# Kernel optimization log

Measured on AMD Instinct MI355X. Metric: run time of the kernel, lower is better.

The kernel has to match this reference:

```python
import jax, jax.numpy as jnp
import numpy as np

B, S, H = 2, 2048, 1024
E, K, F = 64, 8, 512
NORM_TOPK = True
CAP_FACTOR = 2.0


def setup_inputs() -> dict:
    key = jax.random.key(0)
    k0, k1, k2, k3, k4 = jax.random.split(key, 5)
    s_h = 1.0 / np.sqrt(H)
    s_f = 1.0 / np.sqrt(F)
    return {
        "hidden_states": jax.random.normal(k0, (B, S, H), jnp.float32),
        "w_gate": jax.random.normal(k1, (H, E), jnp.float32) * s_h,  # gate: Linear(H->E), no bias
        "w1": jax.random.normal(k2, (E, H, F), jnp.float32) * s_h,   # gate_proj per expert
        "w3": jax.random.normal(k3, (E, H, F), jnp.float32) * s_h,   # up_proj per expert
        "w2": jax.random.normal(k4, (E, F, H), jnp.float32) * s_f,   # down_proj per expert
    }


def reference(hidden_states, w_gate, w1, w3, w2):
    b, s, h = hidden_states.shape
    e = w_gate.shape[1]
    t = b * s
    x = hidden_states.reshape(t, h)
    router_logits = x @ w_gate                                   # [T, E]
    probs = jax.nn.softmax(router_logits.astype(jnp.float32), axis=-1)
    topw, sel = jax.lax.top_k(probs, K)                          # [T, K]
    if NORM_TOPK:
        topw = topw / jnp.sum(topw, axis=-1, keepdims=True)
    topw = topw.astype(x.dtype)

    a = t * K                                                    # total assignments
    c = int(CAP_FACTOR * a / e)                                  # static per-expert capacity
    sel_flat = sel.reshape(a)
    w_flat = topw.reshape(a)
    tok = jnp.repeat(jnp.arange(t), K)
    order = jnp.argsort(sel_flat, stable=True)                   # group assignments by expert
    e_s, t_s, w_s = sel_flat[order], tok[order], w_flat[order]
    counts = jnp.bincount(sel_flat, length=e)
    starts = jnp.cumsum(counts) - counts
    pos = jnp.arange(a) - starts[e_s]                            # position within expert group
    valid = pos < c
    slot = jnp.where(valid, e_s * c + pos, e * c)                # overflow -> dropped sentinel slot

    # dispatch: gather tokens into per-expert contiguous buffer [E, C, H]
    buf = jnp.zeros((e * c + 1, h), x.dtype).at[slot].set(x[t_s])
    xb = buf[: e * c].reshape(e, c, h)
    # grouped gated-SiLU MLP per expert
    g = jnp.einsum('ech,ehf->ecf', xb, w1)
    u = jnp.einsum('ech,ehf->ecf', xb, w3)
    yb = jnp.einsum('ecf,efh->ech', jax.nn.silu(g) * u, w2).reshape(e * c, h)
    # combine: weighted scatter-add back to tokens
    contrib = yb[jnp.minimum(slot, e * c - 1)] * (w_s * valid.astype(x.dtype))[:, None]
    out = jnp.zeros((t, h), x.dtype).at[t_s].add(contrib)
    return out.reshape(b, s, h), router_logits
```

## Files before the change

kernel.cpp:

```cpp
#include <hip/hip_runtime.h>
#include <hip/hip_bf16.h>

#define T_TOK 4096
#define H_DIM 1024
#define E_EXP 64
#define TOPK  8
#define F_DIM 512
#define CAP   1024
#define A_TOT (T_TOK * TOPK)

typedef _Float16 f16;
typedef _Float16 f16x2 __attribute__((ext_vector_type(2)));
typedef _Float16 f16x8 __attribute__((ext_vector_type(8)));
typedef float    f32x4 __attribute__((ext_vector_type(4)));

__global__ __launch_bounds__(256) void pack_w_kernel(
    const float* __restrict__ src, f16* __restrict__ dst, int Kd, int Nd)
{
    const int lane = threadIdx.x & 63;
    const int wv   = threadIdx.x >> 6;
    const int nt_cnt = Nd >> 4, kt_cnt = Kd >> 5;
    int chunk = blockIdx.x * 4 + wv;
    int nt = chunk % nt_cnt;
    int kt = (chunk / nt_cnt) % kt_cnt;
    int e  = chunk / (nt_cnt * kt_cnt);
    const float* s = src + ((size_t)e * Kd + kt * 32 + (lane >> 4) * 8) * Nd
                         + nt * 16 + (lane & 15);
    f16x8 v;
    #pragma unroll
    for (int j = 0; j < 8; ++j) v[j] = (f16)s[(size_t)j * Nd];
    size_t dchunk = ((size_t)e * nt_cnt + nt) * kt_cnt + kt;
    *(f16x8*)(dst + dchunk * 512 + lane * 8) = v;
}

__global__ __launch_bounds__(256) void router_kernel(
    const float* __restrict__ x, const float* __restrict__ wg,
    float* __restrict__ logits_out, int* __restrict__ sel,
    float* __restrict__ wgtA, f16* __restrict__ xh)
{
    __shared__ float xs[16][128];
    __shared__ float ls[16][65];
    const int tid = threadIdx.x;
    const int e  = tid & 63;
    const int tg = tid >> 6;
    const int tb = blockIdx.x * 16;

    float acc[4] = {0.f, 0.f, 0.f, 0.f};
    for (int h0 = 0; h0 < H_DIM; h0 += 128) {
        {
            int r  = tid >> 4;
            int c0 = (tid & 15) * 8;
            const float4* src = (const float4*)(x + (size_t)(tb + r) * H_DIM + h0 + c0);
            float4 v0 = src[0], v1 = src[1];
            *(float4*)&xs[r][c0]     = v0;
            *(float4*)&xs[r][c0 + 4] = v1;
            f16x8 hv;
            hv[0] = (f16)v0.x; hv[1] = (f16)v0.y; hv[2] = (f16)v0.z; hv[3] = (f16)v0.w;
            hv[4] = (f16)v1.x; hv[5] = (f16)v1.y; hv[6] = (f16)v1.z; hv[7] = (f16)v1.w;
            *(f16x8*)(xh + (size_t)(tb + r) * H_DIM + h0 + c0) = hv;
        }
        __syncthreads();
        for (int hh = 0; hh < 128; ++hh) {
            float w = wg[(size_t)(h0 + hh) * E_EXP + e];
            #pragma unroll
            for (int i = 0; i < 4; ++i)
                acc[i] = fmaf(xs[tg * 4 + i][hh], w, acc[i]);
        }
        __syncthreads();
    }
    #pragma unroll
    for (int i = 0; i < 4; ++i) {
        int tt = tg * 4 + i;
        logits_out[(size_t)(tb + tt) * E_EXP + e] = acc[i];
        ls[tt][e] = acc[i];
    }
    __syncthreads();
    if (tid < 16) {
        int tt = tid;
        float lv[8]; int li[8];
        for (int k = 0; k < 8; ++k) {
            float m = -1e30f; int mi = 0;
            for (int j = 0; j < 64; ++j) {
                float v = ls[tt][j];
                if (v > m) { m = v; mi = j; }
            }
            lv[k] = m; li[k] = mi;
            ls[tt][mi] = -1e30f;
        }
        float s = 0.f, wv[8];
        for (int k = 0; k < 8; ++k) { wv[k] = __expf(lv[k] - lv[0]); s += wv[k]; }
        float inv = 1.f / s;
        for (int k = 0; k < 8; ++k) {
            int a = (tb + tt) * TOPK + k;
            sel[a]  = li[k];
            wgtA[a] = wv[k] * inv;
        }
    }
}

__global__ __launch_bounds__(256) void build_lists_kernel(
    const int* __restrict__ sel, const float* __restrict__ wgtA,
    int* __restrict__ tok_list, float* __restrict__ wgt_list,
    int* __restrict__ counts)
{
    __shared__ int sc[256];
    const int e = blockIdx.x;
    const int tid = threadIdx.x;
    const int per = A_TOT / 256;
    const int a0 = tid * per;
    int cnt = 0;
    for (int i = 0; i < per; ++i) cnt += (sel[a0 + i] == e) ? 1 : 0;
    sc[tid] = cnt;
    __syncthreads();
    for (int s = 1; s < 256; s <<= 1) {
        int v = (tid >= s) ? sc[tid - s] : 0;
        __syncthreads();
        sc[tid] += v;
        __syncthreads();
    }
    int total = sc[255];
    int pos = sc[tid] - cnt;
    if (tid == 0) counts[e] = (total < CAP) ? total : CAP;
    for (int i = 0; i < per; ++i) {
        int a = a0 + i;
        if (sel[a] == e) {
            if (pos < CAP) {
                tok_list[e * CAP + pos] = a >> 3;
                wgt_list[e * CAP + pos] = wgtA[a];
            }
            pos++;
        }
    }
}

#define MFMA16(a, b, c) __builtin_amdgcn_mfma_f32_16x16x32_f16(a, b, c, 0, 0, 0)

__global__ __launch_bounds__(256) void gemm1_kernel(
    const f16* __restrict__ xh, const f16* __restrict__ w1p,
    const f16* __restrict__ w3p, const int* __restrict__ tok_list,
    const int* __restrict__ counts, f16* __restrict__ P)
{
    const int id = blockIdx.x;
    const int rest = id >> 3;
    const int g  = (id & 7) + ((rest >> 4) << 3);
    const int m0 = (rest & 15) * 64;
    const int bf = (g & 7) * 64;
    const int e  = g >> 3;
    const int cnt = counts[e];
    if (m0 >= cnt) return;

    __shared__ f16 Xs[64][72];
    __shared__ int tok_s[64];

    const int tid = threadIdx.x;
    const int lane = tid & 63, wv = tid >> 6;
    const int jj = lane & 15, qq = lane >> 4;

    if (tid < 64) {
        int m = m0 + tid;
        tok_s[tid] = (m < cnt) ? tok_list[e * CAP + m] : tok_list[e * CAP];
    }
    __syncthreads();

    const int sr = tid >> 3, sc = (tid & 7) * 8;

    const f16* w1b = w1p + ((size_t)e * 32 + (bf >> 4) + wv) * 32 * 512 + lane * 8;
    const f16* w3b = w3p + ((size_t)e * 32 + (bf >> 4) + wv) * 32 * 512 + lane * 8;

    f32x4 accG[4], accU[4];
    #pragma unroll
    for (int i = 0; i < 4; ++i) {
        accG[i] = (f32x4){0.f, 0.f, 0.f, 0.f};
        accU[i] = (f32x4){0.f, 0.f, 0.f, 0.f};
    }

    f16x8 pG0 = *(const f16x8*)(w1b);
    f16x8 pG1 = *(const f16x8*)(w1b + 512);
    f16x8 pU0 = *(const f16x8*)(w3b);
    f16x8 pU1 = *(const f16x8*)(w3b + 512);

    for (int k0 = 0; k0 < H_DIM; k0 += 64) {
        f16x8 x0 = *(const f16x8*)(xh + (size_t)tok_s[sr]      * H_DIM + k0 + sc);
        f16x8 x1 = *(const f16x8*)(xh + (size_t)tok_s[sr + 32] * H_DIM + k0 + sc);
        __syncthreads();
        *(f16x8*)&Xs[sr][sc]      = x0;
        *(f16x8*)&Xs[sr + 32][sc] = x1;
        __syncthreads();
        f16x8 cG0 = pG0, cG1 = pG1, cU0 = pU0, cU1 = pU1;
        if (k0 + 64 < H_DIM) {
            size_t kg = (size_t)((k0 >> 5) + 2) * 512;
            pG0 = *(const f16x8*)(w1b + kg);
            pG1 = *(const f16x8*)(w1b + kg + 512);
            pU0 = *(const f16x8*)(w3b + kg);
            pU1 = *(const f16x8*)(w3b + kg + 512);
        }
        #pragma unroll
        for (int mt = 0; mt < 4; ++mt) {
            f16x8 a0 = *(const f16x8*)&Xs[mt * 16 + jj][qq * 8];
            f16x8 a1 = *(const f16x8*)&Xs[mt * 16 + jj][32 + qq * 8];
            accG[mt] = MFMA16(a0, cG0, accG[mt]);
            accU[mt] = MFMA16(a0, cU0, accU[mt]);
            accG[mt] = MFMA16(a1, cG1, accG[mt]);
            accU[mt] = MFMA16(a1, cU1, accU[mt]);
        }
    }
    #pragma unroll
    for (int mt = 0; mt < 4; ++mt) {
        #pragma unroll
        for (int r = 0; r < 4; ++r) {
            int row = mt * 16 + qq * 4 + r;
            float gg = accG[mt][r], u = accU[mt][r];
            float p = gg / (1.f + __expf(-gg)) * u;
            P[(size_t)(e * CAP + m0 + row) * F_DIM + bf + wv * 16 + jj] = (f16)p;
        }
    }
}

__global__ __launch_bounds__(256) void gemm2_kernel(
    const f16* __restrict__ P, const f16* __restrict__ w2p,
    const int* __restrict__ tok_list, const float* __restrict__ wgt_list,
    const int* __restrict__ counts, float* __restrict__ out)
{
    const int id = blockIdx.x;
    const int rest = id >> 3;
    const int g  = (id & 7) + ((rest >> 4) << 3);
    const int m0 = (rest & 15) * 64;
    const int h0 = (g & 15) * 64;
    const int e  = g >> 4;
    const int cnt = counts[e];
    if (m0 >= cnt) return;

    __shared__ f16   Ps[64][72];
    __shared__ int   tok_s[64];
    __shared__ float wgt_s[64];

    const int tid = threadIdx.x;
    const int lane = tid & 63, wv = tid >> 6;
    const int jj = lane & 15, qq = lane >> 4;

    if (tid < 64) {
        int m = m0 + tid;
        tok_s[tid] = (m < cnt) ? tok_list[e * CAP + m] : 0;
        wgt_s[tid] = (m < cnt) ? wgt_list[e * CAP + m] : 0.f;
    }

    const int sr = tid >> 3, sc = (tid & 7) * 8;
    const size_t pbase = (size_t)(e * CAP + m0) * F_DIM;

    const f16* w2b = w2p + ((size_t)e * 64 + (h0 >> 4) + wv) * 16 * 512 + lane * 8;

    f32x4 acc[4];
    #pragma unroll
    for (int i = 0; i < 4; ++i) acc[i] = (f32x4){0.f, 0.f, 0.f, 0.f};

    f16x8 p0 = *(const f16x8*)(w2b);
    f16x8 p1 = *(const f16x8*)(w2b + 512);

    for (int k0 = 0; k0 < F_DIM; k0 += 64) {
        f16x8 x0 = *(const f16x8*)(P + pbase + (size_t)sr        * F_DIM + k0 + sc);
        f16x8 x1 = *(const f16x8*)(P + pbase + (size_t)(sr + 32) * F_DIM + k0 + sc);
        __syncthreads();
        *(f16x8*)&Ps[sr][sc]      = x0;
        *(f16x8*)&Ps[sr + 32][sc] = x1;
        __syncthreads();
        f16x8 c0 = p0, c1 = p1;
        if (k0 + 64 < F_DIM) {
            size_t kg = (size_t)((k0 >> 5) + 2) * 512;
            p0 = *(const f16x8*)(w2b + kg);
            p1 = *(const f16x8*)(w2b + kg + 512);
        }
        #pragma unroll
        for (int mt = 0; mt < 4; ++mt) {
            f16x8 a0 = *(const f16x8*)&Ps[mt * 16 + jj][qq * 8];
            f16x8 a1 = *(const f16x8*)&Ps[mt * 16 + jj][32 + qq * 8];
            acc[mt] = MFMA16(a0, c0, acc[mt]);
            acc[mt] = MFMA16(a1, c1, acc[mt]);
        }
    }
    #pragma unroll
    for (int mt = 0; mt < 4; ++mt) {
        #pragma unroll
        for (int r = 0; r < 4; ++r) {
            int row = mt * 16 + qq * 4 + r;
            if (m0 + row < cnt) {
                float y = acc[mt][r] * wgt_s[row];
                unsafeAtomicAdd(&out[(size_t)tok_s[row] * H_DIM + h0 + wv * 16 + jj], y);
            }
        }
    }
}

extern "C" void kernel_launch(void* const* d_in, const int* in_sizes, int n_in,
                              void* d_out, int out_size, void* d_ws, size_t ws_size,
                              hipStream_t stream) {
    const float* x  = (const float*)d_in[0];
    const float* wg = (const float*)d_in[1];
    const float* w1 = (const float*)d_in[2];
    const float* w3 = (const float*)d_in[3];
    const float* w2 = (const float*)d_in[4];

    float* out    = (float*)d_out;
    float* logits = out + (size_t)T_TOK * H_DIM;

    char* ws = (char*)d_ws;
    int*   sel      = (int*)  (ws);
    float* wgtA     = (float*)(ws + (128 << 10));
    int*   tok_list = (int*)  (ws + (256 << 10));
    float* wgt_list = (float*)(ws + (512 << 10));
    int*   counts   = (int*)  (ws + (768 << 10));
    f16*   xh       = (f16*)  (ws + (size_t)(1 << 20));
    f16*   P        = (f16*)  (ws + (size_t)(9 << 20));
    f16*   w1p      = (f16*)  (ws + (size_t)(73 << 20));
    f16*   w3p      = (f16*)  (ws + (size_t)(137 << 20));
    f16*   w2p      = (f16*)  (ws + (size_t)(201 << 20));

    hipMemsetAsync(out, 0, (size_t)T_TOK * H_DIM * sizeof(float), stream);
    pack_w_kernel<<<16384, 256, 0, stream>>>(w1, w1p, H_DIM, F_DIM);
    pack_w_kernel<<<16384, 256, 0, stream>>>(w3, w3p, H_DIM, F_DIM);
    pack_w_kernel<<<16384, 256, 0, stream>>>(w2, w2p, F_DIM, H_DIM);
    router_kernel<<<T_TOK / 16, 256, 0, stream>>>(x, wg, logits, sel, wgtA, xh);
    build_lists_kernel<<<E_EXP, 256, 0, stream>>>(sel, wgtA, tok_list, wgt_list, counts);
    gemm1_kernel<<<16 * 8 * E_EXP, 256, 0, stream>>>(xh, w1p, w3p, tok_list, counts, P);
    gemm2_kernel<<<16 * 16 * E_EXP, 256, 0, stream>>>(P, w2p, tok_list, wgt_list, counts, out);
}
```

Baseline: 742.8 us.

## Coalesce weight packing via LDS tile, double-buffer GEMM tiles, widen gemm2 N-tile

The weight pack kernel now reads rows of the fp32 weights with float4 loads into an LDS tile and transposes them from there, instead of doing strided scalar loads per lane. Both expert GEMMs double-buffer the activation tile in shared memory, which drops one barrier per k-step and overlaps the next global load with the MFMA work. gemm2 now computes a 128-wide output tile per block, with two accumulator sets per wave, halving its grid and the number of times each P tile is reloaded. Block-index decoding is remapped in both GEMMs, which changes how blocks are scheduled; the cost is more registers and LDS per block.

Result: faster. 711.3 us (-4.2%).

```diff
diff --git a/kernel.cpp b/kernel.cpp
--- a/kernel.cpp
+++ b/kernel.cpp
@@ -11,26 +11,44 @@
 
 typedef _Float16 f16;
 typedef _Float16 f16x2 __attribute__((ext_vector_type(2)));
+typedef _Float16 f16x4 __attribute__((ext_vector_type(4)));
 typedef _Float16 f16x8 __attribute__((ext_vector_type(8)));
 typedef float    f32x4 __attribute__((ext_vector_type(4)));
 
 __global__ __launch_bounds__(256) void pack_w_kernel(
     const float* __restrict__ src, f16* __restrict__ dst, int Kd, int Nd)
 {
-    const int lane = threadIdx.x & 63;
-    const int wv   = threadIdx.x >> 6;
-    const int nt_cnt = Nd >> 4, kt_cnt = Kd >> 5;
-    int chunk = blockIdx.x * 4 + wv;
-    int nt = chunk % nt_cnt;
-    int kt = (chunk / nt_cnt) % kt_cnt;
-    int e  = chunk / (nt_cnt * kt_cnt);
-    const float* s = src + ((size_t)e * Kd + kt * 32 + (lane >> 4) * 8) * Nd
-                         + nt * 16 + (lane & 15);
-    f16x8 v;
-    #pragma unroll
-    for (int j = 0; j < 8; ++j) v[j] = (f16)s[(size_t)j * Nd];
-    size_t dchunk = ((size_t)e * nt_cnt + nt) * kt_cnt + kt;
-    *(f16x8*)(dst + dchunk * 512 + lane * 8) = v;
+    __shared__ f16 tile[32][132];
+    const int tid = threadIdx.x;
+    const int nb = Nd >> 7;
+    const int kb = Kd >> 5;
+    const int b = blockIdx.x;
+    const int n0  = (b % nb) * 128;
+    const int kt0 = (b / nb) % kb;
+    const int e   = b / (nb * kb);
+
+    const float* s = src + ((size_t)e * Kd + kt0 * 32) * Nd + n0;
+    #pragma unroll
+    for (int rep = 0; rep < 4; ++rep) {
+        int idx = rep * 256 + tid;
+        int r = idx >> 5, c = (idx & 31) * 4;
+        float4 v = *(const float4*)(s + (size_t)r * Nd + c);
+        f16x4 h; h[0] = (f16)v.x; h[1] = (f16)v.y; h[2] = (f16)v.z; h[3] = (f16)v.w;
+        *(f16x4*)&tile[r][c] = h;
+    }
+    __syncthreads();
+    const int lane = tid & 63, wv = tid >> 6;
+    #pragma unroll
+    for (int ci = 0; ci < 2; ++ci) {
+        int c = wv + ci * 4;
+        f16x8 v;
+        #pragma unroll
+        for (int j = 0; j < 8; ++j)
+            v[j] = tile[(lane >> 4) * 8 + j][c * 16 + (lane & 15)];
+        int nt = (n0 >> 4) + c;
+        size_t chunk = ((size_t)e * (Nd >> 4) + nt) * kb + kt0;
+        *(f16x8*)(dst + chunk * 512 + lane * 8) = v;
+    }
 }
 
 __global__ __launch_bounds__(256) void router_kernel(
@@ -141,31 +159,32 @@
     const int* __restrict__ counts, f16* __restrict__ P)
 {
     const int id = blockIdx.x;
-    const int rest = id >> 3;
-    const int g  = (id & 7) + ((rest >> 4) << 3);
-    const int m0 = (rest & 15) * 64;
-    const int bf = (g & 7) * 64;
-    const int e  = g >> 3;
+    const int x7 = id & 7, r = id >> 3;
+    const int ft = r & 7, mt = (r >> 3) & 15, eh = r >> 7;
+    const int e = x7 + 8 * eh;
     const int cnt = counts[e];
+    const int m0 = mt * 64;
     if (m0 >= cnt) return;
-
-    __shared__ f16 Xs[64][72];
+    const int bf = ft * 64;
+
+    __shared__ f16 Xs[2][64][72];
     __shared__ int tok_s[64];
 
     const int tid = threadIdx.x;
     const int lane = tid & 63, wv = tid >> 6;
     const int jj = lane & 15, qq = lane >> 4;
+    const int sr = tid >> 3, sc = (tid & 7) * 8;
 
     if (tid < 64) {
         int m = m0 + tid;
         tok_s[tid] = (m < cnt) ? tok_list[e * CAP + m] : tok_list[e * CAP];
     }
     __syncthreads();
-
-    const int sr = tid >> 3, sc = (tid & 7) * 8;
-
-    const f16* w1b = w1p + ((size_t)e * 32 + (bf >> 4) + wv) * 32 * 512 + lane * 8;
-    const f16* w3b = w3p + ((size_t)e * 32 + (bf >> 4) + wv) * 32 * 512 + lane * 8;
+    const size_t rowA = (size_t)tok_s[sr] * H_DIM + sc;
+    const size_t rowB = (size_t)tok_s[sr + 32] * H_DIM + sc;
+
+    const f16* w1b = w1p + (((size_t)e * 32 + ft * 4 + wv) * 32) * 512 + lane * 8;
+    const f16* w3b = w3p + (((size_t)e * 32 + ft * 4 + wv) * 32) * 512 + lane * 8;
 
     f32x4 accG[4], accU[4];
     #pragma unroll
@@ -174,42 +193,53 @@
         accU[i] = (f32x4){0.f, 0.f, 0.f, 0.f};
     }
 
-    f16x8 pG0 = *(const f16x8*)(w1b);
-    f16x8 pG1 = *(const f16x8*)(w1b + 512);
-    f16x8 pU0 = *(const f16x8*)(w3b);
-    f16x8 pU1 = *(const f16x8*)(w3b + 512);
-
-    for (int k0 = 0; k0 < H_DIM; k0 += 64) {
-        f16x8 x0 = *(const f16x8*)(xh + (size_t)tok_s[sr]      * H_DIM + k0 + sc);
-        f16x8 x1 = *(const f16x8*)(xh + (size_t)tok_s[sr + 32] * H_DIM + k0 + sc);
-        __syncthreads();
-        *(f16x8*)&Xs[sr][sc]      = x0;
-        *(f16x8*)&Xs[sr + 32][sc] = x1;
-        __syncthreads();
-        f16x8 cG0 = pG0, cG1 = pG1, cU0 = pU0, cU1 = pU1;
-        if (k0 + 64 < H_DIM) {
-            size_t kg = (size_t)((k0 >> 5) + 2) * 512;
-            pG0 = *(const f16x8*)(w1b + kg);
-            pG1 = *(const f16x8*)(w1b + kg + 512);
-            pU0 = *(const f16x8*)(w3b + kg);
-            pU1 = *(const f16x8*)(w3b + kg + 512);
-        }
-        #pragma unroll
-        for (int mt = 0; mt < 4; ++mt) {
-            f16x8 a0 = *(const f16x8*)&Xs[mt * 16 + jj][qq * 8];
-            f16x8 a1 = *(const f16x8*)&Xs[mt * 16 + jj][32 + qq * 8];
-            accG[mt] = MFMA16(a0, cG0, accG[mt]);
-            accU[mt] = MFMA16(a0, cU0, accU[mt]);
-            accG[mt] = MFMA16(a1, cG1, accG[mt]);
-            accU[mt] = MFMA16(a1, cU1, accU[mt]);
-        }
-    }
-    #pragma unroll
-    for (int mt = 0; mt < 4; ++mt) {
-        #pragma unroll
-        for (int r = 0; r < 4; ++r) {
-            int row = mt * 16 + qq * 4 + r;
-            float gg = accG[mt][r], u = accU[mt][r];
+    {
+        f16x8 a = *(const f16x8*)(xh + rowA);
+        f16x8 b = *(const f16x8*)(xh + rowB);
+        *(f16x8*)&Xs[0][sr][sc]      = a;
+        *(f16x8*)&Xs[0][sr + 32][sc] = b;
+    }
+    f16x8 cG0 = *(const f16x8*)(w1b);
+    f16x8 cG1 = *(const f16x8*)(w1b + 512);
+    f16x8 cU0 = *(const f16x8*)(w3b);
+    f16x8 cU1 = *(const f16x8*)(w3b + 512);
+
+    #pragma unroll
+    for (int it = 0; it < 16; ++it) {
+        const int k0 = it * 64;
+        __syncthreads();
+        f16x8 xn0, xn1, nG0, nG1, nU0, nU1;
+        if (it < 15) {
+            xn0 = *(const f16x8*)(xh + rowA + k0 + 64);
+            xn1 = *(const f16x8*)(xh + rowB + k0 + 64);
+            size_t kg = (size_t)(2 * it + 2) * 512;
+            nG0 = *(const f16x8*)(w1b + kg);
+            nG1 = *(const f16x8*)(w1b + kg + 512);
+            nU0 = *(const f16x8*)(w3b + kg);
+            nU1 = *(const f16x8*)(w3b + kg + 512);
+        }
+        const int buf = it & 1;
+        #pragma unroll
+        for (int m2 = 0; m2 < 4; ++m2) {
+            f16x8 a0 = *(const f16x8*)&Xs[buf][m2 * 16 + jj][qq * 8];
+            f16x8 a1 = *(const f16x8*)&Xs[buf][m2 * 16 + jj][32 + qq * 8];
+            accG[m2] = MFMA16(a0, cG0, accG[m2]);
+            accU[m2] = MFMA16(a0, cU0, accU[m2]);
+            accG[m2] = MFMA16(a1, cG1, accG[m2]);
+            accU[m2] = MFMA16(a1, cU1, accU[m2]);
+        }
+        if (it < 15) {
+            *(f16x8*)&Xs[buf ^ 1][sr][sc]      = xn0;
+            *(f16x8*)&Xs[buf ^ 1][sr + 32][sc] = xn1;
+            cG0 = nG0; cG1 = nG1; cU0 = nU0; cU1 = nU1;
+        }
+    }
+    #pragma unroll
+    for (int m2 = 0; m2 < 4; ++m2) {
+        #pragma unroll
+        for (int rr = 0; rr < 4; ++rr) {
+            int row = m2 * 16 + qq * 4 + rr;
+            float gg = accG[m2][rr], u = accU[m2][rr];
             float p = gg / (1.f + __expf(-gg)) * u;
             P[(size_t)(e * CAP + m0 + row) * F_DIM + bf + wv * 16 + jj] = (f16)p;
         }
@@ -222,21 +252,22 @@
     const int* __restrict__ counts, float* __restrict__ out)
 {
     const int id = blockIdx.x;
-    const int rest = id >> 3;
-    const int g  = (id & 7) + ((rest >> 4) << 3);
-    const int m0 = (rest & 15) * 64;
-    const int h0 = (g & 15) * 64;
-    const int e  = g >> 4;
+    const int x7 = id & 7, r = id >> 3;
+    const int ht = r & 7, mt = (r >> 3) & 15, eh = r >> 7;
+    const int e = x7 + 8 * eh;
     const int cnt = counts[e];
+    const int m0 = mt * 64;
     if (m0 >= cnt) return;
-
-    __shared__ f16   Ps[64][72];
+    const int h0 = ht * 128;
+
+    __shared__ f16   Ps[2][64][72];
     __shared__ int   tok_s[64];
     __shared__ float wgt_s[64];
 
     const int tid = threadIdx.x;
     const int lane = tid & 63, wv = tid >> 6;
     const int jj = lane & 15, qq = lane >> 4;
+    const int sr = tid >> 3, sc = (tid & 7) * 8;
 
     if (tid < 64) {
         int m = m0 + tid;
@@ -244,47 +275,68 @@
         wgt_s[tid] = (m < cnt) ? wgt_list[e * CAP + m] : 0.f;
     }
 
-    const int sr = tid >> 3, sc = (tid & 7) * 8;
     const size_t pbase = (size_t)(e * CAP + m0) * F_DIM;
-
-    const f16* w2b = w2p + ((size_t)e * 64 + (h0 >> 4) + wv) * 16 * 512 + lane * 8;
-
-    f32x4 acc[4];
-    #pragma unroll
-    for (int i = 0; i < 4; ++i) acc[i] = (f32x4){0.f, 0.f, 0.f, 0.f};
-
-    f16x8 p0 = *(const f16x8*)(w2b);
-    f16x8 p1 = *(const f16x8*)(w2b + 512);
-
-    for (int k0 = 0; k0 < F_DIM; k0 += 64) {
-        f16x8 x0 = *(const f16x8*)(P + pbase + (size_t)sr        * F_DIM + k0 + sc);
-        f16x8 x1 = *(const f16x8*)(P + pbase + (size_t)(sr + 32) * F_DIM + k0 + sc);
-        __syncthreads();
-        *(f16x8*)&Ps[sr][sc]      = x0;
-        *(f16x8*)&Ps[sr + 32][sc] = x1;
-        __syncthreads();
-        f16x8 c0 = p0, c1 = p1;
-        if (k0 + 64 < F_DIM) {
-            size_t kg = (size_t)((k0 >> 5) + 2) * 512;
-            p0 = *(const f16x8*)(w2b + kg);
-            p1 = *(const f16x8*)(w2b + kg + 512);
-        }
-        #pragma unroll
-        for (int mt = 0; mt < 4; ++mt) {
-            f16x8 a0 = *(const f16x8*)&Ps[mt * 16 + jj][qq * 8];
-            f16x8 a1 = *(const f16x8*)&Ps[mt * 16 + jj][32 + qq * 8];
-            acc[mt] = MFMA16(a0, c0, acc[mt]);
-            acc[mt] = MFMA16(a1, c1, acc[mt]);
-        }
-    }
-    #pragma unroll
-    for (int mt = 0; mt < 4; ++mt) {
-        #pragma unroll
-        for (int r = 0; r < 4; ++r) {
-            int row = mt * 16 + qq * 4 + r;
+    const f16* wA = w2p + (((size_t)e * 64 + ht * 8 + wv) * 16) * 512 + lane * 8;
+    const f16* wB = w2p + (((size_t)e * 64 + ht * 8 + wv + 4) * 16) * 512 + lane * 8;
+
+    f32x4 accA[4], accB[4];
+    #pragma unroll
+    for (int i = 0; i < 4; ++i) {
+        accA[i] = (f32x4){0.f, 0.f, 0.f, 0.f};
+        accB[i] = (f32x4){0.f, 0.f, 0.f, 0.f};
+    }
+
+    {
+        f16x8 a = *(const f16x8*)(P + pbase + (size_t)sr * F_DIM + sc);
+        f16x8 b = *(const f16x8*)(P + pbase + (size_t)(sr + 32) * F_DIM + sc);
+        *(f16x8*)&Ps[0][sr][sc]      = a;
+        *(f16x8*)&Ps[0][sr + 32][sc] = b;
+    }
+    f16x8 cA0 = *(const f16x8*)(wA);
+    f16x8 cA1 = *(const f16x8*)(wA + 512);
+    f16x8 cB0 = *(const f16x8*)(wB);
+    f16x8 cB1 = *(const f16x8*)(wB + 512);
+
+    #pragma unroll
+    for (int it = 0; it < 8; ++it) {
+        const int k0 = it * 64;
+        __syncthreads();
+        f16x8 pn0, pn1, nA0, nA1, nB0, nB1;
+        if (it < 7) {
+            pn0 = *(const f16x8*)(P + pbase + (size_t)sr * F_DIM + k0 + 64 + sc);
+            pn1 = *(const f16x8*)(P + pbase + (size_t)(sr + 32) * F_DIM + k0 + 64 + sc);
+            size_t kg = (size_t)(2 * it + 2) * 512;
+            nA0 = *(const f16x8*)(wA + kg);
+            nA1 = *(const f16x8*)(wA + kg + 512);
+            nB0 = *(const f16x8*)(wB + kg);
+            nB1 = *(const f16x8*)(wB + kg + 512);
+        }
+        const int buf = it & 1;
+        #pragma unroll
+        for (int m2 = 0; m2 < 4; ++m2) {
+            f16x8 a0 = *(const f16x8*)&Ps[buf][m2 * 16 + jj][qq * 8];
+            f16x8 a1 = *(const f16x8*)&Ps[buf][m2 * 16 + jj][32 + qq * 8];
+            accA[m2] = MFMA16(a0, cA0, accA[m2]);
+            accB[m2] = MFMA16(a0, cB0, accB[m2]);
+            accA[m2] = MFMA16(a1, cA1, accA[m2]);
+            accB[m2] = MFMA16(a1, cB1, accB[m2]);
+        }
+        if (it < 7) {
+            *(f16x8*)&Ps[buf ^ 1][sr][sc]      = pn0;
+            *(f16x8*)&Ps[buf ^ 1][sr + 32][sc] = pn1;
+            cA0 = nA0; cA1 = nA1; cB0 = nB0; cB1 = nB1;
+        }
+    }
+    #pragma unroll
+    for (int m2 = 0; m2 < 4; ++m2) {
+        #pragma unroll
+        for (int rr = 0; rr < 4; ++rr) {
+            int row = m2 * 16 + qq * 4 + rr;
             if (m0 + row < cnt) {
-                float y = acc[mt][r] * wgt_s[row];
-                unsafeAtomicAdd(&out[(size_t)tok_s[row] * H_DIM + h0 + wv * 16 + jj], y);
+                float w = wgt_s[row];
+                float* obase = &out[(size_t)tok_s[row] * H_DIM + h0 + wv * 16 + jj];
+                unsafeAtomicAdd(obase,      accA[m2][rr] * w);
+                unsafeAtomicAdd(obase + 64, accB[m2][rr] * w);
             }
         }
     }
@@ -315,11 +367,11 @@
     f16*   w2p      = (f16*)  (ws + (size_t)(201 << 20));
 
     hipMemsetAsync(out, 0, (size_t)T_TOK * H_DIM * sizeof(float), stream);
-    pack_w_kernel<<<16384, 256, 0, stream>>>(w1, w1p, H_DIM, F_DIM);
-    pack_w_kernel<<<16384, 256, 0, stream>>>(w3, w3p, H_DIM, F_DIM);
-    pack_w_kernel<<<16384, 256, 0, stream>>>(w2, w2p, F_DIM, H_DIM);
+    pack_w_kernel<<<8192, 256, 0, stream>>>(w1, w1p, H_DIM, F_DIM);
+    pack_w_kernel<<<8192, 256, 0, stream>>>(w3, w3p, H_DIM, F_DIM);
+    pack_w_kernel<<<8192, 256, 0, stream>>>(w2, w2p, F_DIM, H_DIM);
     router_kernel<<<T_TOK / 16, 256, 0, stream>>>(x, wg, logits, sel, wgtA, xh);
     build_lists_kernel<<<E_EXP, 256, 0, stream>>>(sel, wgtA, tok_list, wgt_list, counts);
-    gemm1_kernel<<<16 * 8 * E_EXP, 256, 0, stream>>>(xh, w1p, w3p, tok_list, counts, P);
-    gemm2_kernel<<<16 * 16 * E_EXP, 256, 0, stream>>>(P, w2p, tok_list, wgt_list, counts, out);
-}
+    gemm1_kernel<<<8192, 256, 0, stream>>>(xh, w1p, w3p, tok_list, counts, P);
+    gemm2_kernel<<<8192, 256, 0, stream>>>(P, w2p, tok_list, wgt_list, counts, out);
+}
```
